# Optimization experiments

Hardware: AMD Instinct MI355X
Metric: run time of the kernel (lower is better)

## Reference

```python
import jax, jax.numpy as jnp
import numpy as np

B, T, C = 2, 2048, 1024
N = 16
D = C // N  # 64


def setup_inputs() -> dict:
    key = jax.random.key(0)
    ks = jax.random.split(key, 5)
    s = 1.0 / np.sqrt(C)  # lecun_normal-ish scale for Dense kernels
    return {
        "src": jax.random.normal(ks[0], (B, T, C), jnp.float32),
        "mask": jnp.ones((B, T), jnp.float32),  # unused on causal path
        "Wq": jax.random.normal(ks[1], (C, C), jnp.float32) * s,
        "bq": jnp.zeros((C,), jnp.float32),
        "Wk": jax.random.normal(ks[2], (C, C), jnp.float32) * s,
        "bk": jnp.zeros((C,), jnp.float32),
        "Wv": jax.random.normal(ks[3], (C, C), jnp.float32) * s,
        "bv": jnp.zeros((C,), jnp.float32),
        "Wo": jax.random.normal(ks[4], (C, C), jnp.float32) * s,
        "bo": jnp.zeros((C,), jnp.float32),
    }


def reference(src, mask, Wq, bq, Wk, bk, Wv, bv, Wo, bo):
    # QKV projections -> [B, N, T, D]
    def heads(x):
        return x.reshape(B, T, N, D).transpose(0, 2, 1, 3)

    q = heads(src @ Wq + bq)
    k = heads(src @ Wk + bk)
    v = heads(src @ Wv + bv)

    # scores [B, N, T, T], causal mask, softmax
    scores = jnp.einsum("bntd,bnsd->bnts", q, k) / jnp.sqrt(jnp.float32(D))
    causal = jnp.tril(jnp.ones((T, T), bool))
    scores = jnp.where(causal, scores, -jnp.inf)
    attn = jax.nn.softmax(scores, axis=-1)

    # weighted values, merge heads, output projection (dropout deterministic)
    out = jnp.einsum("bnts,bnsd->bntd", attn, v)
    out = out.transpose(0, 2, 1, 3).reshape(B, T, C)
    return out @ Wo + bo
```

## Files before the change

### kernel.cpp

```cpp
#include <hip/hip_runtime.h>

typedef __bf16 bf16;
typedef bf16 bf16x8 __attribute__((ext_vector_type(8)));
typedef float f32x4 __attribute__((ext_vector_type(4)));
typedef unsigned short u16;
typedef u16 u16x4 __attribute__((ext_vector_type(4)));
typedef u16 u16x8 __attribute__((ext_vector_type(8)));

typedef const __attribute__((address_space(1))) void* gptr_t;
typedef __attribute__((address_space(3))) void* sptr_t;

__device__ __forceinline__ void async16(const void* g, void* l) {
  __builtin_amdgcn_global_load_lds((gptr_t)g, (sptr_t)l, 16, 0, 0);
}
__device__ __forceinline__ u16 f2bf(float v) {
  return __builtin_bit_cast(u16, (bf16)v);
}

__device__ __forceinline__ size_t paddr(int r, int k, int KT) {
  return (size_t)((r >> 4) * KT + (k >> 5)) * 512 + ((k >> 3) & 3) * 128 +
         (r & 15) * 8 + (k & 7);
}

__global__ void kPrep(const float* __restrict__ src, u16* __restrict__ Xp,
                      const float* __restrict__ Wq, const float* __restrict__ Wk,
                      const float* __restrict__ Wv, const float* __restrict__ Wo,
                      u16* __restrict__ Wp) {
  __shared__ float tile[32][33];
  const int bid = blockIdx.x, tid = threadIdx.x;
  if (bid < 4096) {
    const int i = (bid * 256 + tid) * 4;
    const int m = i >> 10, k = i & 1023;
    float4 v = *(const float4*)&src[i];
    u16x4 o = {f2bf(v.x), f2bf(v.y), f2bf(v.z), f2bf(v.w)};
    *(u16x4*)&Xp[paddr(m, k, 32)] = o;
  } else {
    const int t = bid - 4096;
    const int z = t >> 10, tt = t & 1023;
    const float* W = (z == 0) ? Wq : (z == 1) ? Wk : (z == 2) ? Wv : Wo;
    const int n0 = (tt & 31) * 32, k0 = (tt >> 5) * 32;
    const int tx = tid & 31, ty = tid >> 5;
#pragma unroll
    for (int j = 0; j < 4; ++j)
      tile[ty + j * 8][tx] = W[(size_t)(k0 + ty + j * 8) * 1024 + n0 + tx];
    __syncthreads();
    if (tid < 128) {
      const int sub = tid >> 6, l = tid & 63, hi = l >> 4, lo = l & 15;
      u16x8 o;
#pragma unroll
      for (int e = 0; e < 8; ++e) o[e] = f2bf(tile[hi * 8 + e][sub * 16 + lo]);
      const size_t ad = (size_t)z * 1048576 +
                        (size_t)(((n0 >> 4) + sub) * 32 + (k0 >> 5)) * 512 +
                        hi * 128 + lo * 8;
      *(u16x8*)&Wp[ad] = o;
    }
  }
}

__global__ __launch_bounds__(256, 3) void kGemmQKV(
    const u16* __restrict__ A, const u16* __restrict__ Bt,
    const float* __restrict__ b0, const float* __restrict__ b1,
    const float* __restrict__ b2, u16* __restrict__ outQ) {
  __shared__ __align__(16) u16 Als[2][8 * 512];
  const int tid = threadIdx.x, l = tid & 63, w = tid >> 6;
  const int bid = (blockIdx.x & 7) * 96 + (blockIdx.x >> 3);
  const int mb = bid & 31, nb = bid >> 5;
  const int mbase = mb * 128, nbase = nb * 128;
  const int wr = (w >> 1) * 64, wc = (w & 1) * 64;
  const int hi = l >> 4, lo = l & 15;

  const u16* bb[4];
#pragma unroll
  for (int nf = 0; nf < 4; ++nf)
    bb[nf] = &Bt[(size_t)((nbase + wc + nf * 16) >> 4) * 16384 + l * 8];

  f32x4 acc[4][4];
#pragma unroll
  for (int i = 0; i < 4; ++i)
#pragma unroll
    for (int j = 0; j < 4; ++j) acc[i][j] = (f32x4){0.f, 0.f, 0.f, 0.f};

  auto stageA = [&](int bufi, int kt) {
#pragma unroll
    for (int i = 0; i < 2; ++i) {
      const int fr = w * 2 + i;
      async16(&A[(size_t)((mb * 8 + fr) * 32 + kt) * 512 + l * 8],
              &Als[bufi][fr * 512]);
    }
  };

  bf16x8 breg[2][4];
  stageA(0, 0);
#pragma unroll
  for (int nf = 0; nf < 4; ++nf) breg[0][nf] = *(const bf16x8*)&bb[nf][0];

  auto step = [&](int kt, bf16x8 (&bc)[4], bf16x8 (&bn)[4]) {
    const int cur = kt & 1;
    if (kt < 31) {
      stageA(cur ^ 1, kt + 1);
#pragma unroll
      for (int nf = 0; nf < 4; ++nf)
        bn[nf] = *(const bf16x8*)&bb[nf][(kt + 1) * 512];
      asm volatile("s_waitcnt vmcnt(6)" ::: "memory");
    } else {
      asm volatile("s_waitcnt vmcnt(0)" ::: "memory");
    }
    __builtin_amdgcn_s_barrier();
    __builtin_amdgcn_sched_barrier(0);

    bf16x8 a[4];
#pragma unroll
    for (int mf = 0; mf < 4; ++mf)
      a[mf] = *(const bf16x8*)&Als[cur][((w >> 1) * 4 + mf) * 512 + l * 8];
#pragma unroll
    for (int mf = 0; mf < 4; ++mf)
#pragma unroll
      for (int nf = 0; nf < 4; ++nf)
        acc[mf][nf] = __builtin_amdgcn_mfma_f32_16x16x32_bf16(a[mf], bc[nf],
                                                              acc[mf][nf], 0, 0, 0);
    __builtin_amdgcn_s_barrier();
  };

  for (int kt2 = 0; kt2 < 32; kt2 += 2) {
    step(kt2, breg[0], breg[1]);
    step(kt2 + 1, breg[1], breg[0]);
  }

  u16* Qo = outQ;
  u16* Ko = outQ + 4 * 1048576;
  u16* Vo = outQ + 8 * 1048576;
  const int mat = nb >> 3;
  const float* bias = (mat == 0) ? b0 : (mat == 1) ? b1 : b2;
  const float qs = (mat == 0) ? 0.1803368801f : 1.0f;
#pragma unroll
  for (int nf = 0; nf < 4; ++nf) {
    const int n = nbase + wc + nf * 16 + lo;
    const int cc = n & 1023, h = cc >> 6, d = cc & 63;
    const float bsv = bias[cc];
#pragma unroll
    for (int mf = 0; mf < 4; ++mf)
#pragma unroll
      for (int r = 0; r < 4; ++r) {
        const int m = mbase + wr + mf * 16 + hi * 4 + r;
        const int bb_ = m >> 11, t = m & 2047;
        const u16 hv = f2bf((acc[mf][nf][r] + bsv) * qs);
        const size_t hd = (size_t)(bb_ * 16 + h) * 131072;
        if (mat < 2) {
          (mat == 0 ? Qo : Ko)[hd + paddr(t, d, 2)] = hv;
        } else {
          Vo[hd + paddr(d, t, 64)] = hv;
        }
      }
  }
}

__global__ __launch_bounds__(256, 2) void kGemmO(
    const u16* __restrict__ A, const u16* __restrict__ Bt,
    const float* __restrict__ b0, float* __restrict__ outF) {
  __shared__ __align__(16) u16 Als[2][8 * 512];
  const int tid = threadIdx.x, l = tid & 63, w = tid >> 6;
  const int bid = (blockIdx.x & 7) * 64 + (blockIdx.x >> 3);
  const int mb = bid & 31, nb = bid >> 5;
  const int mbase = mb * 128, nbase = nb * 64;
  const int wr = (w >> 1) * 64, wc = (w & 1) * 32;
  const int hi = l >> 4, lo = l & 15;

  const u16* bb[2];
#pragma unroll
  for (int nf = 0; nf < 2; ++nf)
    bb[nf] = &Bt[(size_t)((nbase + wc + nf * 16) >> 4) * 16384 + l * 8];

  f32x4 acc[4][2];
#pragma unroll
  for (int i = 0; i < 4; ++i)
#pragma unroll
    for (int j = 0; j < 2; ++j) acc[i][j] = (f32x4){0.f, 0.f, 0.f, 0.f};

  auto stageA = [&](int bufi, int kt) {
#pragma unroll
    for (int i = 0; i < 2; ++i) {
      const int fr = w * 2 + i;
      async16(&A[(size_t)((mb * 8 + fr) * 32 + kt) * 512 + l * 8],
              &Als[bufi][fr * 512]);
    }
  };

  bf16x8 breg[2][2];
  stageA(0, 0);
#pragma unroll
  for (int nf = 0; nf < 2; ++nf) breg[0][nf] = *(const bf16x8*)&bb[nf][0];

  auto step = [&](int kt, bf16x8 (&bc)[2], bf16x8 (&bn)[2]) {
    const int cur = kt & 1;
    if (kt < 31) {
      stageA(cur ^ 1, kt + 1);
#pragma unroll
      for (int nf = 0; nf < 2; ++nf)
        bn[nf] = *(const bf16x8*)&bb[nf][(kt + 1) * 512];
      asm volatile("s_waitcnt vmcnt(4)" ::: "memory");
    } else {
      asm volatile("s_waitcnt vmcnt(0)" ::: "memory");
    }
    __builtin_amdgcn_s_barrier();
    __builtin_amdgcn_sched_barrier(0);

    bf16x8 a[4];
#pragma unroll
    for (int mf = 0; mf < 4; ++mf)
      a[mf] = *(const bf16x8*)&Als[cur][((w >> 1) * 4 + mf) * 512 + l * 8];
#pragma unroll
    for (int mf = 0; mf < 4; ++mf)
#pragma unroll
      for (int nf = 0; nf < 2; ++nf)
        acc[mf][nf] = __builtin_amdgcn_mfma_f32_16x16x32_bf16(a[mf], bc[nf],
                                                              acc[mf][nf], 0, 0, 0);
    __builtin_amdgcn_s_barrier();
  };

  for (int kt2 = 0; kt2 < 32; kt2 += 2) {
    step(kt2, breg[0], breg[1]);
    step(kt2 + 1, breg[1], breg[0]);
  }

#pragma unroll
  for (int nf = 0; nf < 2; ++nf) {
    const int n = nbase + wc + nf * 16 + lo;
    const float bsv = b0[n];
#pragma unroll
    for (int mf = 0; mf < 4; ++mf)
#pragma unroll
      for (int r = 0; r < 4; ++r) {
        const int m = mbase + wr + mf * 16 + hi * 4 + r;
        outF[(size_t)m * 1024 + n] = acc[mf][nf][r] + bsv;
      }
  }
}

#define PSTR 88
__global__ __launch_bounds__(256, 2) void kAttn(const u16* __restrict__ Qp,
                                                const u16* __restrict__ Kp,
                                                const u16* __restrict__ Vp,
                                                u16* __restrict__ AOp) {
  __shared__ __align__(16) u16 Pl[4][16 * PSTR];
  const int tid = threadIdx.x, l = tid & 63, w = tid >> 6;
  const int g = l >> 4, c = l & 15;
  const int pi = blockIdx.x, bh = blockIdx.y;
  const int qtA = pi, qtB = 31 - pi;
  const size_t head = (size_t)bh * 131072;
  const u16* Kh = Kp + head;
  const u16* Vh = Vp + head;

  bf16x8 aqA[2], aqB[2];
#pragma unroll
  for (int ks = 0; ks < 2; ++ks) {
    aqA[ks] = *(const bf16x8*)&Qp[head + (size_t)((qtA * 4 + w) * 2 + ks) * 512 + l * 8];
    aqB[ks] = *(const bf16x8*)&Qp[head + (size_t)((qtB * 4 + w) * 2 + ks) * 512 + l * 8];
  }

  f32x4 accA[4], accB[4];
#pragma unroll
  for (int i = 0; i < 4; ++i) {
    accA[i] = (f32x4){0.f, 0.f, 0.f, 0.f};
    accB[i] = (f32x4){0.f, 0.f, 0.f, 0.f};
  }
  float lA_ = 0.f, lB_ = 0.f;

  bf16x8 kr[8], vr[8];
#pragma unroll
  for (int f = 0; f < 8; ++f)
    kr[f] = *(const bf16x8*)&Kh[(size_t)f * 512 + l * 8];

  auto finishTile = [&](const f32x4* sT, bool diag, f32x4* accO, float& lpart) {
    float v[16];
#pragma unroll
    for (int nf = 0; nf < 4; ++nf)
#pragma unroll
      for (int r = 0; r < 4; ++r) v[nf * 4 + r] = sT[nf][r];
    if (diag) {
      const int qg = w * 16 + c;
#pragma unroll
      for (int nf = 0; nf < 4; ++nf)
#pragma unroll
        for (int r = 0; r < 4; ++r)
          if (nf * 16 + g * 4 + r > qg) v[nf * 4 + r] = -__builtin_inff();
    }
    float p[16];
#pragma unroll
    for (int i = 0; i < 16; ++i) p[i] = __builtin_exp2f(v[i]);
#pragma unroll
    for (int nf = 0; nf < 4; ++nf) {
      u16x4 q4 = {f2bf(p[nf * 4 + 0]), f2bf(p[nf * 4 + 1]),
                  f2bf(p[nf * 4 + 2]), f2bf(p[nf * 4 + 3])};
      *(u16x4*)&Pl[w][c * PSTR + nf * 16 + g * 4] = q4;
    }
    float s0 = (p[0] + p[1]) + (p[2] + p[3]);
    float s1 = (p[4] + p[5]) + (p[6] + p[7]);
    float s2 = (p[8] + p[9]) + (p[10] + p[11]);
    float s3 = (p[12] + p[13]) + (p[14] + p[15]);
    lpart += (s0 + s1) + (s2 + s3);
#pragma unroll
    for (int ks2 = 0; ks2 < 2; ++ks2) {
      bf16x8 pf = *(const bf16x8*)&Pl[w][c * PSTR + ks2 * 32 + g * 8];
#pragma unroll
      for (int nd = 0; nd < 4; ++nd)
        accO[nd] = __builtin_amdgcn_mfma_f32_16x16x32_bf16(pf, vr[nd * 2 + ks2],
                                                           accO[nd], 0, 0, 0);
    }
  };

  for (int st = 0; st <= qtB; ++st) {
#pragma unroll
    for (int f = 0; f < 8; ++f)
      vr[f] = *(const bf16x8*)&Vh[(size_t)((f >> 1) * 64 + st * 2 + (f & 1)) * 512 +
                                  l * 8];
    const bool pair = (st <= qtA);
    f32x4 sB[4], sA[4];
#pragma unroll
    for (int i = 0; i < 4; ++i) {
      sB[i] = (f32x4){0.f, 0.f, 0.f, 0.f};
      sA[i] = (f32x4){0.f, 0.f, 0.f, 0.f};
    }
#pragma unroll
    for (int nf = 0; nf < 4; ++nf)
#pragma unroll
      for (int ks = 0; ks < 2; ++ks)
        sB[nf] = __builtin_amdgcn_mfma_f32_16x16x32_bf16(kr[nf * 2 + ks], aqB[ks],
                                                         sB[nf], 0, 0, 0);
    if (pair)
#pragma unroll
      for (int nf = 0; nf < 4; ++nf)
#pragma unroll
        for (int ks = 0; ks < 2; ++ks)
          sA[nf] = __builtin_amdgcn_mfma_f32_16x16x32_bf16(kr[nf * 2 + ks], aqA[ks],
                                                           sA[nf], 0, 0, 0);
    if (st < qtB) {
#pragma unroll
      for (int f = 0; f < 8; ++f)
        kr[f] = *(const bf16x8*)&Kh[(size_t)((st + 1) * 8 + f) * 512 + l * 8];
    }
    finishTile(sB, st == qtB, accB, lB_);
    if (pair) finishTile(sA, st == qtA, accA, lA_);
  }

  const int b = bh >> 4, h = bh & 15;
  auto writeOut = [&](int qt, f32x4* accO, float lpart) {
    float lc = lpart + __shfl_xor(lpart, 16);
    lc += __shfl_xor(lc, 32);
#pragma unroll
    for (int r = 0; r < 4; ++r) {
      const float lr = __shfl(lc, g * 4 + r);
      const float rin = 1.0f / lr;
      const int mg = b * 2048 + qt * 64 + w * 16 + g * 4 + r;
#pragma unroll
      for (int nd = 0; nd < 4; ++nd) {
        const int col = h * 64 + nd * 16 + c;
        AOp[paddr(mg, col, 32)] = f2bf(accO[nd][r] * rin);
      }
    }
  };
  writeOut(qtA, accA, lA_);
  writeOut(qtB, accB, lB_);
}

extern "C" void kernel_launch(void* const* d_in, const int* in_sizes, int n_in,
                              void* d_out, int out_size, void* d_ws, size_t ws_size,
                              hipStream_t stream) {
  const float* src = (const float*)d_in[0];
  const float* Wq = (const float*)d_in[2];
  const float* bq = (const float*)d_in[3];
  const float* Wk = (const float*)d_in[4];
  const float* bk = (const float*)d_in[5];
  const float* Wv = (const float*)d_in[6];
  const float* bv = (const float*)d_in[7];
  const float* Wo = (const float*)d_in[8];
  const float* bo = (const float*)d_in[9];
  float* out = (float*)d_out;

  char* ws = (char*)d_ws;
  u16* Wp = (u16*)(ws);
  u16* Xp = (u16*)(ws + 8ull * 1024 * 1024);
  u16* Qb = (u16*)(ws + 16ull * 1024 * 1024);
  u16* AOp = (u16*)(ws + 40ull * 1024 * 1024);

  kPrep<<<dim3(8192), dim3(256), 0, stream>>>(src, Xp, Wq, Wk, Wv, Wo, Wp);
  kGemmQKV<<<dim3(768), dim3(256), 0, stream>>>(Xp, Wp, bq, bk, bv, Qb);
  kAttn<<<dim3(16, 32), dim3(256), 0, stream>>>(Qb, Qb + 4 * 1048576,
                                                Qb + 8 * 1048576, AOp);
  kGemmO<<<dim3(512), dim3(256), 0, stream>>>(AOp, Wp + 3ull * 1048576, bo, out);
}
```

Measured before the change: 115.3 us.

## Split paired query-tile attention blocks into one block per query tile

The attention kernel previously paired query tiles qt and 31-qt in one block so that each K/V tile load served two query tiles and the work per block was balanced. Now each block handles a single query tile, the grid doubles to 32x32, and launch bounds raise occupancy to 4 blocks per SM. The aim is more parallelism and lower register pressure. In exchange, K/V loads are no longer shared between two query tiles, and per-block work becomes uneven, with the heaviest tiles launched first.

```diff
diff --git a/kernel.cpp b/kernel.cpp
--- a/kernel.cpp
+++ b/kernel.cpp
@@ -237,46 +237,60 @@
 }
 
 #define PSTR 88
-__global__ __launch_bounds__(256, 2) void kAttn(const u16* __restrict__ Qp,
+__global__ __launch_bounds__(256, 4) void kAttn(const u16* __restrict__ Qp,
                                                 const u16* __restrict__ Kp,
                                                 const u16* __restrict__ Vp,
                                                 u16* __restrict__ AOp) {
   __shared__ __align__(16) u16 Pl[4][16 * PSTR];
   const int tid = threadIdx.x, l = tid & 63, w = tid >> 6;
   const int g = l >> 4, c = l & 15;
-  const int pi = blockIdx.x, bh = blockIdx.y;
-  const int qtA = pi, qtB = 31 - pi;
+  const int qt = 31 - blockIdx.x;
+  const int bh = blockIdx.y;
   const size_t head = (size_t)bh * 131072;
   const u16* Kh = Kp + head;
   const u16* Vh = Vp + head;
 
-  bf16x8 aqA[2], aqB[2];
-#pragma unroll
-  for (int ks = 0; ks < 2; ++ks) {
-    aqA[ks] = *(const bf16x8*)&Qp[head + (size_t)((qtA * 4 + w) * 2 + ks) * 512 + l * 8];
-    aqB[ks] = *(const bf16x8*)&Qp[head + (size_t)((qtB * 4 + w) * 2 + ks) * 512 + l * 8];
-  }
-
-  f32x4 accA[4], accB[4];
-#pragma unroll
-  for (int i = 0; i < 4; ++i) {
-    accA[i] = (f32x4){0.f, 0.f, 0.f, 0.f};
-    accB[i] = (f32x4){0.f, 0.f, 0.f, 0.f};
-  }
-  float lA_ = 0.f, lB_ = 0.f;
+  bf16x8 aq[2];
+#pragma unroll
+  for (int ks = 0; ks < 2; ++ks)
+    aq[ks] = *(const bf16x8*)&Qp[head + (size_t)((qt * 4 + w) * 2 + ks) * 512 + l * 8];
+
+  f32x4 accO[4];
+#pragma unroll
+  for (int i = 0; i < 4; ++i) accO[i] = (f32x4){0.f, 0.f, 0.f, 0.f};
+  float l_ = 0.f;
 
   bf16x8 kr[8], vr[8];
 #pragma unroll
   for (int f = 0; f < 8; ++f)
     kr[f] = *(const bf16x8*)&Kh[(size_t)f * 512 + l * 8];
 
-  auto finishTile = [&](const f32x4* sT, bool diag, f32x4* accO, float& lpart) {
+  for (int st = 0; st <= qt; ++st) {
+#pragma unroll
+    for (int f = 0; f < 8; ++f)
+      vr[f] = *(const bf16x8*)&Vh[(size_t)((f >> 1) * 64 + st * 2 + (f & 1)) * 512 +
+                                  l * 8];
+    f32x4 sT[4];
+#pragma unroll
+    for (int i = 0; i < 4; ++i) sT[i] = (f32x4){0.f, 0.f, 0.f, 0.f};
+#pragma unroll
+    for (int nf = 0; nf < 4; ++nf)
+#pragma unroll
+      for (int ks = 0; ks < 2; ++ks)
+        sT[nf] = __builtin_amdgcn_mfma_f32_16x16x32_bf16(kr[nf * 2 + ks], aq[ks],
+                                                         sT[nf], 0, 0, 0);
+    if (st < qt) {
+#pragma unroll
+      for (int f = 0; f < 8; ++f)
+        kr[f] = *(const bf16x8*)&Kh[(size_t)((st + 1) * 8 + f) * 512 + l * 8];
+    }
+
     float v[16];
 #pragma unroll
     for (int nf = 0; nf < 4; ++nf)
 #pragma unroll
       for (int r = 0; r < 4; ++r) v[nf * 4 + r] = sT[nf][r];
-    if (diag) {
+    if (st == qt) {
       const int qg = w * 16 + c;
 #pragma unroll
       for (int nf = 0; nf < 4; ++nf)
@@ -284,6 +298,7 @@
         for (int r = 0; r < 4; ++r)
           if (nf * 16 + g * 4 + r > qg) v[nf * 4 + r] = -__builtin_inff();
     }
+
     float p[16];
 #pragma unroll
     for (int i = 0; i < 16; ++i) p[i] = __builtin_exp2f(v[i]);
@@ -297,7 +312,8 @@
     float s1 = (p[4] + p[5]) + (p[6] + p[7]);
     float s2 = (p[8] + p[9]) + (p[10] + p[11]);
     float s3 = (p[12] + p[13]) + (p[14] + p[15]);
-    lpart += (s0 + s1) + (s2 + s3);
+    l_ += (s0 + s1) + (s2 + s3);
+
 #pragma unroll
     for (int ks2 = 0; ks2 < 2; ++ks2) {
       bf16x8 pf = *(const bf16x8*)&Pl[w][c * PSTR + ks2 * 32 + g * 8];
@@ -306,60 +322,22 @@
         accO[nd] = __builtin_amdgcn_mfma_f32_16x16x32_bf16(pf, vr[nd * 2 + ks2],
                                                            accO[nd], 0, 0, 0);
     }
-  };
-
-  for (int st = 0; st <= qtB; ++st) {
-#pragma unroll
-    for (int f = 0; f < 8; ++f)
-      vr[f] = *(const bf16x8*)&Vh[(size_t)((f >> 1) * 64 + st * 2 + (f & 1)) * 512 +
-                                  l * 8];
-    const bool pair = (st <= qtA);
-    f32x4 sB[4], sA[4];
-#pragma unroll
-    for (int i = 0; i < 4; ++i) {
-      sB[i] = (f32x4){0.f, 0.f, 0.f, 0.f};
-      sA[i] = (f32x4){0.f, 0.f, 0.f, 0.f};
-    }
-#pragma unroll
-    for (int nf = 0; nf < 4; ++nf)
-#pragma unroll
-      for (int ks = 0; ks < 2; ++ks)
-        sB[nf] = __builtin_amdgcn_mfma_f32_16x16x32_bf16(kr[nf * 2 + ks], aqB[ks],
-                                                         sB[nf], 0, 0, 0);
-    if (pair)
-#pragma unroll
-      for (int nf = 0; nf < 4; ++nf)
-#pragma unroll
-        for (int ks = 0; ks < 2; ++ks)
-          sA[nf] = __builtin_amdgcn_mfma_f32_16x16x32_bf16(kr[nf * 2 + ks], aqA[ks],
-                                                           sA[nf], 0, 0, 0);
-    if (st < qtB) {
-#pragma unroll
-      for (int f = 0; f < 8; ++f)
-        kr[f] = *(const bf16x8*)&Kh[(size_t)((st + 1) * 8 + f) * 512 + l * 8];
-    }
-    finishTile(sB, st == qtB, accB, lB_);
-    if (pair) finishTile(sA, st == qtA, accA, lA_);
   }
 
   const int b = bh >> 4, h = bh & 15;
-  auto writeOut = [&](int qt, f32x4* accO, float lpart) {
-    float lc = lpart + __shfl_xor(lpart, 16);
-    lc += __shfl_xor(lc, 32);
-#pragma unroll
-    for (int r = 0; r < 4; ++r) {
-      const float lr = __shfl(lc, g * 4 + r);
-      const float rin = 1.0f / lr;
-      const int mg = b * 2048 + qt * 64 + w * 16 + g * 4 + r;
-#pragma unroll
-      for (int nd = 0; nd < 4; ++nd) {
-        const int col = h * 64 + nd * 16 + c;
-        AOp[paddr(mg, col, 32)] = f2bf(accO[nd][r] * rin);
-      }
-    }
-  };
-  writeOut(qtA, accA, lA_);
-  writeOut(qtB, accB, lB_);
+  float lc = l_ + __shfl_xor(l_, 16);
+  lc += __shfl_xor(lc, 32);
+#pragma unroll
+  for (int r = 0; r < 4; ++r) {
+    const float lr = __shfl(lc, g * 4 + r);
+    const float rin = 1.0f / lr;
+    const int mg = b * 2048 + qt * 64 + w * 16 + g * 4 + r;
+#pragma unroll
+    for (int nd = 0; nd < 4; ++nd) {
+      const int col = h * 64 + nd * 16 + c;
+      AOp[paddr(mg, col, 32)] = f2bf(accO[nd][r] * rin);
+    }
+  }
 }
 
 extern "C" void kernel_launch(void* const* d_in, const int* in_sizes, int n_in,
@@ -384,7 +362,7 @@
 
   kPrep<<<dim3(8192), dim3(256), 0, stream>>>(src, Xp, Wq, Wk, Wv, Wo, Wp);
   kGemmQKV<<<dim3(768), dim3(256), 0, stream>>>(Xp, Wp, bq, bk, bv, Qb);
-  kAttn<<<dim3(16, 32), dim3(256), 0, stream>>>(Qb, Qb + 4 * 1048576,
+  kAttn<<<dim3(32, 32), dim3(256), 0, stream>>>(Qb, Qb + 4 * 1048576,
                                                 Qb + 8 * 1048576, AOp);
   kGemmO<<<dim3(512), dim3(256), 0, stream>>>(AOp, Wp + 3ull * 1048576, bo, out);
 }
```

Measured after the change: 138.9 us. 1.2x slower.

## Share V tiles across waves via double-buffered async LDS staging

Applied to the files above, without the earlier changes.

Each of the four waves used to load the full V tile straight from global memory into registers every iteration. V tiles are now fetched cooperatively with async global-to-LDS loads, each wave bringing in two fragments, into a double buffer that is prefetched one step ahead. Waves then read the fragments from LDS. This cuts redundant global V traffic by a factor of four and hides the load latency behind the QK and softmax work. In exchange it adds LDS use, which may affect occupancy, plus a vmcnt wait and a block-wide barrier on every iteration.

```diff
diff --git a/kernel.cpp b/kernel.cpp
--- a/kernel.cpp
+++ b/kernel.cpp
@@ -241,6 +241,7 @@
                                                 const u16* __restrict__ Kp,
                                                 const u16* __restrict__ Vp,
                                                 u16* __restrict__ AOp) {
+  __shared__ __align__(16) u16 Vls[2][8 * 512];
   __shared__ __align__(16) u16 Pl[4][16 * PSTR];
   const int tid = threadIdx.x, l = tid & 63, w = tid >> 6;
   const int g = l >> 4, c = l & 15;
@@ -265,12 +266,25 @@
   }
   float lA_ = 0.f, lB_ = 0.f;
 
-  bf16x8 kr[8], vr[8];
+  auto stageV = [&](int buf, int st) {
+#pragma unroll
+    for (int i = 0; i < 2; ++i) {
+      const int fr = w * 2 + i;
+      async16(&Vh[(size_t)((fr >> 1) * 64 + st * 2 + (fr & 1)) * 512 + l * 8],
+              &Vls[buf][fr * 512]);
+    }
+  };
+
+  bf16x8 kr[8];
 #pragma unroll
   for (int f = 0; f < 8; ++f)
     kr[f] = *(const bf16x8*)&Kh[(size_t)f * 512 + l * 8];
-
-  auto finishTile = [&](const f32x4* sT, bool diag, f32x4* accO, float& lpart) {
+  stageV(0, 0);
+  asm volatile("s_waitcnt vmcnt(0)" ::: "memory");
+  __builtin_amdgcn_s_barrier();
+
+  auto finishTile = [&](const f32x4* sT, bool diag, f32x4* accO, float& lpart,
+                        const bf16x8* vf) {
     float v[16];
 #pragma unroll
     for (int nf = 0; nf < 4; ++nf)
@@ -303,17 +317,16 @@
       bf16x8 pf = *(const bf16x8*)&Pl[w][c * PSTR + ks2 * 32 + g * 8];
 #pragma unroll
       for (int nd = 0; nd < 4; ++nd)
-        accO[nd] = __builtin_amdgcn_mfma_f32_16x16x32_bf16(pf, vr[nd * 2 + ks2],
+        accO[nd] = __builtin_amdgcn_mfma_f32_16x16x32_bf16(pf, vf[nd * 2 + ks2],
                                                            accO[nd], 0, 0, 0);
     }
   };
 
   for (int st = 0; st <= qtB; ++st) {
-#pragma unroll
-    for (int f = 0; f < 8; ++f)
-      vr[f] = *(const bf16x8*)&Vh[(size_t)((f >> 1) * 64 + st * 2 + (f & 1)) * 512 +
-                                  l * 8];
+    const int cur = st & 1;
+    if (st < qtB) stageV(cur ^ 1, st + 1);
     const bool pair = (st <= qtA);
+
     f32x4 sB[4], sA[4];
 #pragma unroll
     for (int i = 0; i < 4; ++i) {
@@ -338,8 +351,17 @@
       for (int f = 0; f < 8; ++f)
         kr[f] = *(const bf16x8*)&Kh[(size_t)((st + 1) * 8 + f) * 512 + l * 8];
     }
-    finishTile(sB, st == qtB, accB, lB_);
-    if (pair) finishTile(sA, st == qtA, accA, lA_);
+    bf16x8 vf[8];
+#pragma unroll
+    for (int f = 0; f < 8; ++f)
+      vf[f] = *(const bf16x8*)&Vls[cur][f * 512 + l * 8];
+
+    finishTile(sB, st == qtB, accB, lB_, vf);
+    if (pair) finishTile(sA, st == qtA, accA, lA_, vf);
+
+    asm volatile("s_waitcnt vmcnt(8)" ::: "memory");
+    __builtin_amdgcn_s_barrier();
+    __builtin_amdgcn_sched_barrier(0);
   }
 
   const int b = bh >> 4, h = bh & 15;
```

New measurement: 116.8 us. About the same (+1.3%).

## Split attention key tiles across wave pairs with LDS reduction of partial outputs

Applied to the files above, without the earlier changes.

The attention kernel now launches 512 threads per block. Each pair of waves shares one 16-row query group, and each wave handles half of every 64-key tile. Partial output accumulators and row sums are combined through shared memory at the end, and one wave of each pair writes the result. This doubles the waves available per block to hide latency and cuts per-wave registers. The cost is an extra LDS reduction, block-wide syncs, more shared memory, and half the threads sitting idle during the output write.

```diff
diff --git a/kernel.cpp b/kernel.cpp
--- a/kernel.cpp
+++ b/kernel.cpp
@@ -236,13 +236,16 @@
   }
 }
 
-#define PSTR 88
-__global__ __launch_bounds__(256, 2) void kAttn(const u16* __restrict__ Qp,
+#define PSTR 36
+__global__ __launch_bounds__(512, 4) void kAttn(const u16* __restrict__ Qp,
                                                 const u16* __restrict__ Kp,
                                                 const u16* __restrict__ Vp,
                                                 u16* __restrict__ AOp) {
-  __shared__ __align__(16) u16 Pl[4][16 * PSTR];
+  __shared__ __align__(16) u16 Pl[8][16 * PSTR];
+  __shared__ __align__(16) float Red[4][2][16][64];
+  __shared__ float RedL[4][2][64];
   const int tid = threadIdx.x, l = tid & 63, w = tid >> 6;
+  const int grp = w >> 1, half = w & 1;
   const int g = l >> 4, c = l & 15;
   const int pi = blockIdx.x, bh = blockIdx.y;
   const int qtA = pi, qtB = 31 - pi;
@@ -253,8 +256,8 @@
   bf16x8 aqA[2], aqB[2];
 #pragma unroll
   for (int ks = 0; ks < 2; ++ks) {
-    aqA[ks] = *(const bf16x8*)&Qp[head + (size_t)((qtA * 4 + w) * 2 + ks) * 512 + l * 8];
-    aqB[ks] = *(const bf16x8*)&Qp[head + (size_t)((qtB * 4 + w) * 2 + ks) * 512 + l * 8];
+    aqA[ks] = *(const bf16x8*)&Qp[head + (size_t)((qtA * 4 + grp) * 2 + ks) * 512 + l * 8];
+    aqB[ks] = *(const bf16x8*)&Qp[head + (size_t)((qtB * 4 + grp) * 2 + ks) * 512 + l * 8];
   }
 
   f32x4 accA[4], accB[4];
@@ -265,101 +268,122 @@
   }
   float lA_ = 0.f, lB_ = 0.f;
 
-  bf16x8 kr[8], vr[8];
-#pragma unroll
-  for (int f = 0; f < 8; ++f)
-    kr[f] = *(const bf16x8*)&Kh[(size_t)f * 512 + l * 8];
+  bf16x8 kr[4];
+#pragma unroll
+  for (int f = 0; f < 4; ++f)
+    kr[f] = *(const bf16x8*)&Kh[(size_t)((half * 2 + (f >> 1)) * 2 + (f & 1)) * 512 + l * 8];
+  bf16x8 vr[4];
 
   auto finishTile = [&](const f32x4* sT, bool diag, f32x4* accO, float& lpart) {
-    float v[16];
-#pragma unroll
-    for (int nf = 0; nf < 4; ++nf)
-#pragma unroll
-      for (int r = 0; r < 4; ++r) v[nf * 4 + r] = sT[nf][r];
+    float v[8];
+#pragma unroll
+    for (int sf = 0; sf < 2; ++sf)
+#pragma unroll
+      for (int r = 0; r < 4; ++r) v[sf * 4 + r] = sT[sf][r];
     if (diag) {
-      const int qg = w * 16 + c;
-#pragma unroll
-      for (int nf = 0; nf < 4; ++nf)
+      const int qin = grp * 16 + c;
+#pragma unroll
+      for (int sf = 0; sf < 2; ++sf)
 #pragma unroll
         for (int r = 0; r < 4; ++r)
-          if (nf * 16 + g * 4 + r > qg) v[nf * 4 + r] = -__builtin_inff();
-    }
-    float p[16];
-#pragma unroll
-    for (int i = 0; i < 16; ++i) p[i] = __builtin_exp2f(v[i]);
-#pragma unroll
-    for (int nf = 0; nf < 4; ++nf) {
-      u16x4 q4 = {f2bf(p[nf * 4 + 0]), f2bf(p[nf * 4 + 1]),
-                  f2bf(p[nf * 4 + 2]), f2bf(p[nf * 4 + 3])};
-      *(u16x4*)&Pl[w][c * PSTR + nf * 16 + g * 4] = q4;
-    }
-    float s0 = (p[0] + p[1]) + (p[2] + p[3]);
-    float s1 = (p[4] + p[5]) + (p[6] + p[7]);
-    float s2 = (p[8] + p[9]) + (p[10] + p[11]);
-    float s3 = (p[12] + p[13]) + (p[14] + p[15]);
-    lpart += (s0 + s1) + (s2 + s3);
-#pragma unroll
-    for (int ks2 = 0; ks2 < 2; ++ks2) {
-      bf16x8 pf = *(const bf16x8*)&Pl[w][c * PSTR + ks2 * 32 + g * 8];
-#pragma unroll
-      for (int nd = 0; nd < 4; ++nd)
-        accO[nd] = __builtin_amdgcn_mfma_f32_16x16x32_bf16(pf, vr[nd * 2 + ks2],
-                                                           accO[nd], 0, 0, 0);
-    }
+          if (half * 32 + sf * 16 + g * 4 + r > qin) v[sf * 4 + r] = -__builtin_inff();
+    }
+    float p[8];
+#pragma unroll
+    for (int i = 0; i < 8; ++i) p[i] = __builtin_exp2f(v[i]);
+#pragma unroll
+    for (int sf = 0; sf < 2; ++sf) {
+      u16x4 q4 = {f2bf(p[sf * 4 + 0]), f2bf(p[sf * 4 + 1]),
+                  f2bf(p[sf * 4 + 2]), f2bf(p[sf * 4 + 3])};
+      *(u16x4*)&Pl[w][c * PSTR + sf * 16 + g * 4] = q4;
+    }
+    lpart += ((p[0] + p[1]) + (p[2] + p[3])) + ((p[4] + p[5]) + (p[6] + p[7]));
+    bf16x8 pf = *(const bf16x8*)&Pl[w][c * PSTR + g * 8];
+#pragma unroll
+    for (int nd = 0; nd < 4; ++nd)
+      accO[nd] = __builtin_amdgcn_mfma_f32_16x16x32_bf16(pf, vr[nd], accO[nd], 0, 0, 0);
   };
 
   for (int st = 0; st <= qtB; ++st) {
 #pragma unroll
-    for (int f = 0; f < 8; ++f)
-      vr[f] = *(const bf16x8*)&Vh[(size_t)((f >> 1) * 64 + st * 2 + (f & 1)) * 512 +
-                                  l * 8];
+    for (int nd = 0; nd < 4; ++nd)
+      vr[nd] = *(const bf16x8*)&Vh[(size_t)(nd * 64 + st * 2 + half) * 512 + l * 8];
     const bool pair = (st <= qtA);
-    f32x4 sB[4], sA[4];
-#pragma unroll
-    for (int i = 0; i < 4; ++i) {
+
+    f32x4 sB[2], sA[2];
+#pragma unroll
+    for (int i = 0; i < 2; ++i) {
       sB[i] = (f32x4){0.f, 0.f, 0.f, 0.f};
       sA[i] = (f32x4){0.f, 0.f, 0.f, 0.f};
     }
 #pragma unroll
-    for (int nf = 0; nf < 4; ++nf)
+    for (int sf = 0; sf < 2; ++sf)
 #pragma unroll
       for (int ks = 0; ks < 2; ++ks)
-        sB[nf] = __builtin_amdgcn_mfma_f32_16x16x32_bf16(kr[nf * 2 + ks], aqB[ks],
-                                                         sB[nf], 0, 0, 0);
+        sB[sf] = __builtin_amdgcn_mfma_f32_16x16x32_bf16(kr[sf * 2 + ks], aqB[ks],
+                                                         sB[sf], 0, 0, 0);
     if (pair)
 #pragma unroll
-      for (int nf = 0; nf < 4; ++nf)
+      for (int sf = 0; sf < 2; ++sf)
 #pragma unroll
         for (int ks = 0; ks < 2; ++ks)
-          sA[nf] = __builtin_amdgcn_mfma_f32_16x16x32_bf16(kr[nf * 2 + ks], aqA[ks],
-                                                           sA[nf], 0, 0, 0);
+          sA[sf] = __builtin_amdgcn_mfma_f32_16x16x32_bf16(kr[sf * 2 + ks], aqA[ks],
+                                                           sA[sf], 0, 0, 0);
     if (st < qtB) {
 #pragma unroll
-      for (int f = 0; f < 8; ++f)
-        kr[f] = *(const bf16x8*)&Kh[(size_t)((st + 1) * 8 + f) * 512 + l * 8];
+      for (int f = 0; f < 4; ++f)
+        kr[f] = *(const bf16x8*)&Kh[(size_t)(((st + 1) * 4 + half * 2 + (f >> 1)) * 2 +
+                                             (f & 1)) * 512 + l * 8];
     }
     finishTile(sB, st == qtB, accB, lB_);
     if (pair) finishTile(sA, st == qtA, accA, lA_);
   }
 
-  const int b = bh >> 4, h = bh & 15;
-  auto writeOut = [&](int qt, f32x4* accO, float lpart) {
-    float lc = lpart + __shfl_xor(lpart, 16);
-    lc += __shfl_xor(lc, 32);
-#pragma unroll
-    for (int r = 0; r < 4; ++r) {
-      const float lr = __shfl(lc, g * 4 + r);
-      const float rin = 1.0f / lr;
-      const int mg = b * 2048 + qt * 64 + w * 16 + g * 4 + r;
-#pragma unroll
-      for (int nd = 0; nd < 4; ++nd) {
-        const int col = h * 64 + nd * 16 + c;
-        AOp[paddr(mg, col, 32)] = f2bf(accO[nd][r] * rin);
+  float lcB = lB_ + __shfl_xor(lB_, 16);
+  lcB += __shfl_xor(lcB, 32);
+  float lcA = lA_ + __shfl_xor(lA_, 16);
+  lcA += __shfl_xor(lcA, 32);
+  __syncthreads();
+  if (half) {
+#pragma unroll
+    for (int nd = 0; nd < 4; ++nd)
+#pragma unroll
+      for (int r = 0; r < 4; ++r) {
+        Red[grp][0][nd * 4 + r][l] = accB[nd][r];
+        Red[grp][1][nd * 4 + r][l] = accA[nd][r];
       }
-    }
-  };
-  writeOut(qtA, accA, lA_);
-  writeOut(qtB, accB, lB_);
+    RedL[grp][0][l] = lcB;
+    RedL[grp][1][l] = lcA;
+  }
+  __syncthreads();
+  if (!half) {
+#pragma unroll
+    for (int nd = 0; nd < 4; ++nd)
+#pragma unroll
+      for (int r = 0; r < 4; ++r) {
+        accB[nd][r] += Red[grp][0][nd * 4 + r][l];
+        accA[nd][r] += Red[grp][1][nd * 4 + r][l];
+      }
+    lcB += RedL[grp][0][l];
+    lcA += RedL[grp][1][l];
+
+    const int b = bh >> 4, h = bh & 15;
+    auto writeOut = [&](int qt, f32x4* accO, float lc) {
+#pragma unroll
+      for (int r = 0; r < 4; ++r) {
+        const float lr = __shfl(lc, g * 4 + r);
+        const float rin = 1.0f / lr;
+        const int mg = b * 2048 + qt * 64 + grp * 16 + g * 4 + r;
+#pragma unroll
+        for (int nd = 0; nd < 4; ++nd) {
+          const int col = h * 64 + nd * 16 + c;
+          AOp[paddr(mg, col, 32)] = f2bf(accO[nd][r] * rin);
+        }
+      }
+    };
+    writeOut(qtB, accB, lcB);
+    writeOut(qtA, accA, lcA);
+  }
 }
 
 extern "C" void kernel_launch(void* const* d_in, const int* in_sizes, int n_in,
@@ -384,7 +408,7 @@
 
   kPrep<<<dim3(8192), dim3(256), 0, stream>>>(src, Xp, Wq, Wk, Wv, Wo, Wp);
   kGemmQKV<<<dim3(768), dim3(256), 0, stream>>>(Xp, Wp, bq, bk, bv, Qb);
-  kAttn<<<dim3(16, 32), dim3(256), 0, stream>>>(Qb, Qb + 4 * 1048576,
+  kAttn<<<dim3(16, 32), dim3(512), 0, stream>>>(Qb, Qb + 4 * 1048576,
                                                 Qb + 8 * 1048576, AOp);
   kGemmO<<<dim3(512), dim3(256), 0, stream>>>(AOp, Wp + 3ull * 1048576, bo, out);
 }
```

New measurement: 116.7 us. Within noise of the previous version (+1.2%).
